# Performance work log

Hardware: AMD Instinct MI355X
Metric: run time of the kernel (lower is better)

The kernel has to match this reference:

```python
import jax, jax.numpy as jnp
import numpy as np

N_NODES = 50000
N_EDGES = 800000
N_GRAPHS = 128
IN_DIM = 12          # state_ndim + action_ndim
C = 64               # n_channels
N_LAYERS = 2
NEG_SLOPE = 0.01     # torch leaky_relu default


def setup_inputs() -> dict:
    key = jax.random.key(0)
    ks = jax.random.split(key, 16)
    state = jax.random.normal(ks[0], (N_NODES, 8), dtype=jnp.float32)
    action = jax.random.normal(ks[1], (N_NODES, 4), dtype=jnp.float32)
    edge_index = jax.random.randint(ks[2], (2, N_EDGES), 0, N_NODES, dtype=jnp.int64)
    edge_attr = jax.random.normal(ks[3], (N_EDGES, IN_DIM), dtype=jnp.float32)
    batch = jnp.sort(jax.random.randint(ks[4], (N_NODES,), 0, N_GRAPHS, dtype=jnp.int64))
    s = 0.05
    params = {
        "W_in": jax.random.normal(ks[5], (IN_DIM, C), dtype=jnp.float32) * s,
        "b_in": jnp.zeros((C,), dtype=jnp.float32),
        "W_self": jax.random.normal(ks[6], (N_LAYERS, C, C), dtype=jnp.float32) * s,
        "W_nbr": jax.random.normal(ks[7], (N_LAYERS, C, C), dtype=jnp.float32) * s,
        "W_edge": jax.random.normal(ks[8], (N_LAYERS, IN_DIM, C), dtype=jnp.float32) * s,
        "b_conv": jnp.zeros((N_LAYERS, C), dtype=jnp.float32),
        "W_out": jax.random.normal(ks[9], (C, 1), dtype=jnp.float32) * s,
        "b_out": jnp.zeros((1,), dtype=jnp.float32),
    }
    return {"state": state, "action": action, "edge_index": edge_index,
            "edge_attr": edge_attr, "batch": batch, **params}


def reference(state, action, edge_index, edge_attr, batch,
              W_in, b_in, W_self, W_nbr, W_edge, b_conv, W_out, b_out):
    N = state.shape[0]
    src, dst = edge_index[0], edge_index[1]
    act = lambda v: jax.nn.leaky_relu(v, NEG_SLOPE)

    # read-in: concat state/action -> node embedding [N, C]
    x = jnp.concatenate([state, action], axis=-1)
    h = act(x @ W_in + b_in)

    # message passing: gather -> transform -> scatter-add, edge_attr-conditioned
    for l in range(W_self.shape[0]):
        m = h[src] @ W_nbr[l] + edge_attr @ W_edge[l]          # [E, C]
        agg = jax.ops.segment_sum(m, dst, num_segments=N)      # [N, C]
        h = act(h @ W_self[l] + agg + b_conv[l])

    # read-out to scalar per node, then scatter_mean over graph ids
    y = h @ W_out + b_out                                      # [N, 1]
    sums = jax.ops.segment_sum(y, batch, num_segments=N_GRAPHS)
    counts = jax.ops.segment_sum(jnp.ones((N, 1), y.dtype), batch,
                                 num_segments=N_GRAPHS)
    return sums / jnp.maximum(counts, 1.0)                     # [B, 1]
```

## Files before the change

### kernel.cpp

```cpp
#include <hip/hip_runtime.h>

#define NN 50000
#define NE 800000
#define NG 128
#define IN_DIM 12
#define C 64
#define NEG_SLOPE 0.01f
#define SCAN_BLOCKS 196
#define NOWN 8
#define OWN_RANGE 6250
#define ESTRIPE 2048
#define NSTRIPES ((NE + ESTRIPE - 1) / ESTRIPE)

typedef short short8 __attribute__((ext_vector_type(8)));
typedef float f32x4 __attribute__((ext_vector_type(4)));
typedef unsigned int uint4v __attribute__((ext_vector_type(4)));

__device__ __forceinline__ float lrelu(float v) {
    return v > 0.f ? v : NEG_SLOPE * v;
}
__device__ __forceinline__ float bflo(uint32_t v) { return __uint_as_float(v << 16); }
__device__ __forceinline__ float bfhi(uint32_t v) { return __uint_as_float(v & 0xffff0000u); }
__device__ __forceinline__ unsigned short bf16r(float x) {
    uint32_t u = __float_as_uint(x);
    u += 0x7fffu + ((u >> 16) & 1u);
    return (unsigned short)(u >> 16);
}
__device__ __forceinline__ uint32_t pack_bf16(float lo, float hi) {
    return (uint32_t)bf16r(lo) | ((uint32_t)bf16r(hi) << 16);
}

__global__ void readin_kernel(const float* __restrict__ state,
                              const float* __restrict__ action,
                              const float* __restrict__ W_in,
                              const float* __restrict__ b_in,
                              uint32_t* __restrict__ hb) {
    __shared__ float sW[IN_DIM * C];
    __shared__ float sb[C];
    int tid = threadIdx.x;
    for (int i = tid; i < IN_DIM * C; i += blockDim.x) sW[i] = W_in[i];
    if (tid < C) sb[tid] = b_in[tid];
    __syncthreads();

    int node = blockIdx.x * (blockDim.x >> 6) + (tid >> 6);
    int c = tid & 63;
    if (node >= NN) return;

    float x[IN_DIM];
#pragma unroll
    for (int k = 0; k < 8; k++) x[k] = state[node * 8 + k];
#pragma unroll
    for (int k = 0; k < 4; k++) x[8 + k] = action[node * 4 + k];

    float acc = sb[c];
#pragma unroll
    for (int k = 0; k < IN_DIM; k++) acc += x[k] * sW[k * C + c];
    float res = lrelu(acc);
    float p = __shfl_xor(res, 1);
    if (!(c & 1)) hb[node * 32 + (c >> 1)] = pack_bf16(res, p);
}

__global__ void hist_part(const int* __restrict__ dst, int* __restrict__ deg) {
    int owner = blockIdx.x & (NOWN - 1);
    int stripe = blockIdx.x >> 3;
    int lo = owner * OWN_RANGE, hi = lo + OWN_RANGE;
    int base = stripe * ESTRIPE;
    int end = base + ESTRIPE; if (end > NE) end = NE;
    for (int e = base + threadIdx.x; e < end; e += 256) {
        int d = dst[e];
        if (d >= lo && d < hi) atomicAdd(&deg[d], 1);
    }
}

__global__ void scan1_kernel(const int* __restrict__ deg,
                             int* __restrict__ excl,
                             int* __restrict__ bsum) {
    __shared__ int tmp[256];
    int tid = threadIdx.x;
    int i = blockIdx.x * 256 + tid;
    int v = (i < NN) ? deg[i] : 0;
    tmp[tid] = v;
    __syncthreads();
    for (int off = 1; off < 256; off <<= 1) {
        int t = (tid >= off) ? tmp[tid - off] : 0;
        __syncthreads();
        tmp[tid] += t;
        __syncthreads();
    }
    if (i < NN) excl[i] = tmp[tid] - v;
    if (tid == 255) bsum[blockIdx.x] = tmp[255];
}

__global__ void scan23_kernel(const int* __restrict__ excl,
                              const int* __restrict__ bsum,
                              int* __restrict__ row_start,
                              int* __restrict__ cursor) {
    __shared__ int s_off;
    int tid = threadIdx.x;
    if (tid < 64) {
        int p = 0;
        for (int i = tid; i < blockIdx.x; i += 64) p += bsum[i];
#pragma unroll
        for (int off = 32; off; off >>= 1) p += __shfl_xor(p, off);
        if (tid == 0) s_off = p;
    }
    __syncthreads();
    int i = blockIdx.x * 256 + tid;
    if (i < NN) {
        int v = excl[i] + s_off;
        row_start[i] = v;
        cursor[i] = v;
    }
}

__global__ void fill_part(const int* __restrict__ src,
                          const int* __restrict__ dst,
                          int* __restrict__ cursor,
                          int2* __restrict__ csr2) {
    int owner = blockIdx.x & (NOWN - 1);
    int stripe = blockIdx.x >> 3;
    int lo = owner * OWN_RANGE, hi = lo + OWN_RANGE;
    int base = stripe * ESTRIPE;
    int end = base + ESTRIPE; if (end > NE) end = NE;
    for (int e = base + threadIdx.x; e < end; e += 256) {
        int d = dst[e];
        if (d >= lo && d < hi) {
            int slot = atomicAdd(&cursor[d], 1);
            csr2[slot] = make_int2(src[e], e);
        }
    }
}

__global__ void wprep_kernel(const float* __restrict__ W_self,
                             const float* __restrict__ W_nbr,
                             unsigned short* __restrict__ WT) {
    int idx = blockIdx.x * 256 + threadIdx.x;
    if (idx >= 2 * 64 * 128) return;
    int l = idx >> 13;
    int rem = idx & 8191;
    int col = rem >> 7;
    int k = rem & 127;
    float v = (k < C) ? W_self[l * C * C + k * C + col]
                      : W_nbr[l * C * C + (k - C) * C + col];
    WT[idx] = bf16r(v);
}

__global__ void agg_e_kernel(const float* __restrict__ edge_attr,
                             const int* __restrict__ row_start,
                             const int* __restrict__ deg,
                             const int2* __restrict__ csr2,
                             const float* __restrict__ W_edge,
                             const float* __restrict__ b_conv,
                             float* __restrict__ E0,
                             float* __restrict__ E1) {
    __shared__ float sWe0[IN_DIM * C];
    __shared__ float sWe1[IN_DIM * C];
    __shared__ float sb0[C];
    __shared__ float sb1[C];
    int tid = threadIdx.x;
    for (int i = tid; i < IN_DIM * C; i += blockDim.x) {
        sWe0[i] = W_edge[i];
        sWe1[i] = W_edge[IN_DIM * C + i];
    }
    if (tid < C) { sb0[tid] = b_conv[tid]; sb1[tid] = b_conv[C + tid]; }
    __syncthreads();

    int node = blockIdx.x * (blockDim.x >> 6) + (tid >> 6);
    int lane = tid & 63;
    int g = lane >> 4;
    int cc = lane & 15;
    if (node >= NN) return;
    int start = row_start[node], cnt = deg[node];

    int myeid = (lane < cnt) ? csr2[start + lane].y : 0;
    int nb = cnt < 64 ? cnt : 64;

    float acc = 0.f, acc2 = 0.f;
    int j = 0;
    for (; j + 8 <= nb; j += 8) {
        int e0 = __shfl(myeid, j + g);
        int e1 = __shfl(myeid, j + 4 + g);
        if (cc < IN_DIM) {
            acc  += edge_attr[e0 * IN_DIM + cc];
            acc2 += edge_attr[e1 * IN_DIM + cc];
        }
    }
    for (; j + 4 <= nb; j += 4) {
        int e0 = __shfl(myeid, j + g);
        if (cc < IN_DIM) acc += edge_attr[e0 * IN_DIM + cc];
    }
    {
        int e0 = __shfl(myeid, (j + g < 64) ? (j + g) : 0);
        if (j + g < nb && cc < IN_DIM) acc += edge_attr[e0 * IN_DIM + cc];
    }
    for (int i2 = 64 + g; i2 < cnt; i2 += 4) {
        int e = csr2[start + i2].y;
        if (cc < IN_DIM) acc += edge_attr[e * IN_DIM + cc];
    }
    acc += acc2;
    acc += __shfl_xor(acc, 16);
    acc += __shfl_xor(acc, 32);
    float e0v = sb0[lane];
    float e1v = sb1[lane];
#pragma unroll
    for (int k = 0; k < IN_DIM; k++) {
        float ak = __shfl(acc, k);
        e0v += ak * sWe0[k * C + lane];
        e1v += ak * sWe1[k * C + lane];
    }
    E0[node * C + lane] = e0v;
    E1[node * C + lane] = e1v;
}

__global__ void gather_kernel(const uint32_t* __restrict__ hb_in,
                              const int* __restrict__ row_start,
                              const int* __restrict__ deg,
                              const int2* __restrict__ csr2,
                              uint32_t* __restrict__ aggb) {
    int tid = threadIdx.x;
    int node = blockIdx.x * (blockDim.x >> 6) + (tid >> 6);
    int lane = tid & 63;
    if (node >= NN) return;

    int start = row_start[node], cnt = deg[node];
    int half = lane >> 5;
    int q = lane & 31;

    int myidx = (lane < cnt) ? csr2[start + lane].x : 0;
    int nb = cnt < 64 ? cnt : 64;

    float a0 = 0.f, a1 = 0.f, b0v = 0.f, b1v = 0.f;
    float c0 = 0.f, c1 = 0.f, d0 = 0.f, d1 = 0.f;
    int j = 0;
    for (; j + 16 <= nb; j += 16) {
        int p = j + 4 * half;
        int s0 = __shfl(myidx, p);
        int s1 = __shfl(myidx, p + 1);
        int s2 = __shfl(myidx, p + 2);
        int s3 = __shfl(myidx, p + 3);
        int s4 = __shfl(myidx, p + 8);
        int s5 = __shfl(myidx, p + 9);
        int s6 = __shfl(myidx, p + 10);
        int s7 = __shfl(myidx, p + 11);
        uint32_t v0 = hb_in[s0 * 32 + q];
        uint32_t v1 = hb_in[s1 * 32 + q];
        uint32_t v2 = hb_in[s2 * 32 + q];
        uint32_t v3 = hb_in[s3 * 32 + q];
        uint32_t v4 = hb_in[s4 * 32 + q];
        uint32_t v5 = hb_in[s5 * 32 + q];
        uint32_t v6 = hb_in[s6 * 32 + q];
        uint32_t v7 = hb_in[s7 * 32 + q];
        a0  += bflo(v0); a1  += bfhi(v0);
        b0v += bflo(v1); b1v += bfhi(v1);
        c0  += bflo(v2); c1  += bfhi(v2);
        d0  += bflo(v3); d1  += bfhi(v3);
        a0  += bflo(v4); a1  += bfhi(v4);
        b0v += bflo(v5); b1v += bfhi(v5);
        c0  += bflo(v6); c1  += bfhi(v6);
        d0  += bflo(v7); d1  += bfhi(v7);
    }
    for (; j + 8 <= nb; j += 8) {
        int p = j + 4 * half;
        int s0 = __shfl(myidx, p);
        int s1 = __shfl(myidx, p + 1);
        int s2 = __shfl(myidx, p + 2);
        int s3 = __shfl(myidx, p + 3);
        uint32_t v0 = hb_in[s0 * 32 + q];
        uint32_t v1 = hb_in[s1 * 32 + q];
        uint32_t v2 = hb_in[s2 * 32 + q];
        uint32_t v3 = hb_in[s3 * 32 + q];
        a0  += bflo(v0); a1  += bfhi(v0);
        b0v += bflo(v1); b1v += bfhi(v1);
        c0  += bflo(v2); c1  += bfhi(v2);
        d0  += bflo(v3); d1  += bfhi(v3);
    }
    for (; j + 2 <= nb; j += 2) {
        int s = __shfl(myidx, j + half);
        uint32_t v = hb_in[s * 32 + q];
        a0 += bflo(v); a1 += bfhi(v);
    }
    {
        int s = __shfl(myidx, (j < 64) ? j : 0);
        if (j < nb && half == 0) {
            uint32_t v = hb_in[s * 32 + q];
            a0 += bflo(v); a1 += bfhi(v);
        }
    }
    for (int i2 = 64 + half; i2 < cnt; i2 += 2) {
        int s = csr2[start + i2].x;
        uint32_t v = hb_in[s * 32 + q];
        a0 += bflo(v); a1 += bfhi(v);
    }
    a0 += b0v + c0 + d0;
    a1 += b1v + c1 + d1;
    a0 += __shfl_xor(a0, 32);
    a1 += __shfl_xor(a1, 32);
    if (lane < 32) aggb[node * 32 + q] = pack_bf16(a0, a1);
}

__global__ __launch_bounds__(512) void gemm_kernel(
        const uint32_t* __restrict__ hbA,
        const uint32_t* __restrict__ aggb,
        const unsigned short* __restrict__ WT,
        const float* __restrict__ E,
        unsigned short* __restrict__ hb_out) {
    int tid = threadIdx.x;
    int w = tid >> 6;
    int l = tid & 63;
    int mt = blockIdx.x * 2 + (w >> 2);
    if (mt * 16 >= NN) return;
    int nt = w & 3;
    int node_base = mt * 16;

    int arow = l & 15;
    int kg = l >> 4;
    int gcol = nt * 16 + arow;

    const uint32_t* aptr = hbA + (node_base + arow) * 32 + kg * 4;
    const uint32_t* gptr = aggb + (node_base + arow) * 32 + kg * 4;
    short8 a0 = __builtin_bit_cast(short8, *reinterpret_cast<const uint4v*>(aptr));
    short8 a1 = __builtin_bit_cast(short8, *reinterpret_cast<const uint4v*>(aptr + 16));
    short8 a2 = __builtin_bit_cast(short8, *reinterpret_cast<const uint4v*>(gptr));
    short8 a3 = __builtin_bit_cast(short8, *reinterpret_cast<const uint4v*>(gptr + 16));

    const unsigned short* bbase = WT + gcol * 128 + kg * 8;
    short8 b0 = __builtin_bit_cast(short8, *reinterpret_cast<const uint4v*>(bbase));
    short8 b1 = __builtin_bit_cast(short8, *reinterpret_cast<const uint4v*>(bbase + 32));
    short8 b2 = __builtin_bit_cast(short8, *reinterpret_cast<const uint4v*>(bbase + 64));
    short8 b3 = __builtin_bit_cast(short8, *reinterpret_cast<const uint4v*>(bbase + 96));

    f32x4 acc;
#pragma unroll
    for (int r = 0; r < 4; r++)
        acc[r] = E[(node_base + kg * 4 + r) * C + gcol];

    acc = __builtin_amdgcn_mfma_f32_16x16x32_bf16(a0, b0, acc, 0, 0, 0);
    acc = __builtin_amdgcn_mfma_f32_16x16x32_bf16(a1, b1, acc, 0, 0, 0);
    acc = __builtin_amdgcn_mfma_f32_16x16x32_bf16(a2, b2, acc, 0, 0, 0);
    acc = __builtin_amdgcn_mfma_f32_16x16x32_bf16(a3, b3, acc, 0, 0, 0);

#pragma unroll
    for (int r = 0; r < 4; r++) {
        float res = lrelu(acc[r]);
        hb_out[(node_base + kg * 4 + r) * C + gcol] = bf16r(res);
    }
}

__global__ void readout_fused(const unsigned short* __restrict__ hb,
                              const float* __restrict__ W_out,
                              const float* __restrict__ b_out,
                              const int* __restrict__ batch,
                              float* __restrict__ sums,
                              float* __restrict__ counts) {
    __shared__ float s_sum[NG];
    __shared__ float s_cnt[NG];
    int tid = threadIdx.x;
    if (tid < NG) { s_sum[tid] = 0.f; s_cnt[tid] = 0.f; }
    __syncthreads();

    int lane = tid & 63;
    int wave = tid >> 6;
    int base = blockIdx.x * 256 + wave * 64;
    float w = W_out[lane];
    float b0 = b_out[0];

    if (base < NN) {
        int last = base + 63;
        bool full = (last < NN);
        int gf = batch[base];
        int gl = batch[full ? last : (NN - 1)];
        if (full && gf == gl) {
            float p = 0.f;
            for (int i = 0; i < 64; i++)
                p += __uint_as_float((uint32_t)hb[(base + i) * C + lane] << 16);
            p *= w;
#pragma unroll
            for (int off = 32; off; off >>= 1) p += __shfl_xor(p, off);
            if (lane == 0) {
                atomicAdd(&s_sum[gf], p + 64.f * b0);
                atomicAdd(&s_cnt[gf], 64.f);
            }
        } else {
            float y_local = 0.f;
            for (int i = 0; i < 64; i++) {
                int nd = base + i;
                float v = 0.f;
                if (nd < NN) v = __uint_as_float((uint32_t)hb[nd * C + lane] << 16) * w;
#pragma unroll
                for (int off = 32; off; off >>= 1) v += __shfl_xor(v, off);
                if (lane == i) y_local = v + b0;
            }
            int nd = base + lane;
            if (nd < NN) {
                int g = batch[nd];
                atomicAdd(&s_sum[g], y_local);
                atomicAdd(&s_cnt[g], 1.0f);
            }
        }
    }
    __syncthreads();
    if (tid < NG && s_cnt[tid] != 0.f) {
        atomicAdd(&sums[tid], s_sum[tid]);
        atomicAdd(&counts[tid], s_cnt[tid]);
    }
}

__global__ void finalize_kernel(const float* __restrict__ sums,
                                const float* __restrict__ counts,
                                float* __restrict__ out) {
    int g = threadIdx.x;
    if (g < NG) out[g] = sums[g] / fmaxf(counts[g], 1.0f);
}

extern "C" void kernel_launch(void* const* d_in, const int* in_sizes, int n_in,
                              void* d_out, int out_size, void* d_ws, size_t ws_size,
                              hipStream_t stream) {
    const float* state     = (const float*)d_in[0];
    const float* action    = (const float*)d_in[1];
    const int*   edge_index= (const int*)d_in[2];
    const float* edge_attr = (const float*)d_in[3];
    const int*   batch     = (const int*)d_in[4];
    const float* W_in      = (const float*)d_in[5];
    const float* b_in      = (const float*)d_in[6];
    const float* W_self    = (const float*)d_in[7];
    const float* W_nbr     = (const float*)d_in[8];
    const float* W_edge    = (const float*)d_in[9];
    const float* b_conv    = (const float*)d_in[10];
    const float* W_out     = (const float*)d_in[11];
    const float* b_out     = (const float*)d_in[12];
    float* out = (float*)d_out;

    const int* src = edge_index;
    const int* dst = edge_index + NE;

    float* ws      = (float*)d_ws;
    float* E0      = ws;
    float* E1      = E0 + NN * C;
    float* sums    = E1 + NN * C;
    float* counts  = sums + NG;
    int*   deg     = (int*)(counts + NG);
    int*   excl    = deg + NN;
    int*   row_start = excl + NN;
    int*   cursor  = row_start + NN;
    int*   bsum    = cursor + NN;
    int2*  csr2    = (int2*)(bsum + 256);
    uint32_t* hb_a = (uint32_t*)(csr2 + NE);
    uint32_t* hb_b = hb_a + NN * 32;
    uint32_t* aggb = hb_b + NN * 32;
    unsigned short* WT = (unsigned short*)(aggb + NN * 32);

    hipMemsetAsync(deg, 0, NN * sizeof(int), stream);
    hipMemsetAsync(sums, 0, 2 * NG * sizeof(float), stream);

    const int THREADS = 256;
    int node_blocks = (NN + 3) / 4;
    int part_blocks = NSTRIPES * NOWN;

    readin_kernel<<<node_blocks, THREADS, 0, stream>>>(state, action, W_in, b_in, hb_a);

    hist_part<<<part_blocks, THREADS, 0, stream>>>(dst, deg);
    scan1_kernel<<<SCAN_BLOCKS, 256, 0, stream>>>(deg, excl, bsum);
    scan23_kernel<<<SCAN_BLOCKS, 256, 0, stream>>>(excl, bsum, row_start, cursor);
    fill_part<<<part_blocks, THREADS, 0, stream>>>(src, dst, cursor, csr2);

    wprep_kernel<<<64, 256, 0, stream>>>(W_self, W_nbr, WT);

    agg_e_kernel<<<node_blocks, THREADS, 0, stream>>>(
        edge_attr, row_start, deg, csr2, W_edge, b_conv, E0, E1);

    int gemm_blocks = (3125 + 1) / 2;

    gather_kernel<<<node_blocks, THREADS, 0, stream>>>(hb_a, row_start, deg, csr2, aggb);
    gemm_kernel<<<gemm_blocks, 512, 0, stream>>>(
        hb_a, aggb, WT, E0, (unsigned short*)hb_b);

    gather_kernel<<<node_blocks, THREADS, 0, stream>>>(hb_b, row_start, deg, csr2, aggb);
    gemm_kernel<<<gemm_blocks, 512, 0, stream>>>(
        hb_b, aggb, WT + 64 * 128, E1, (unsigned short*)hb_a);

    int ro_blocks = (NN + 255) / 256;
    readout_fused<<<ro_blocks, THREADS, 0, stream>>>(
        (const unsigned short*)hb_a, W_out, b_out, batch, sums, counts);
    finalize_kernel<<<1, 128, 0, stream>>>(sums, counts, out);
}
```

Measured before the change: 338.2 us.

## Fold edge-attribute projection into MFMA GEMM via bf16 CSR-ordered edge features

fill_part now converts each edge's 12 attributes to bf16 and writes them into a 32-byte record in CSR order, next to a separate source-index array. agg_e only sums these contiguous records per node into a 12-wide bf16 aggregate. The W_edge projection and bias move into the GEMM as a fifth MFMA step over an extended K dimension of 160. This removes the random edge_attr gather and the two fp32 [N,64] E buffers, at the cost of a larger CSR write in fill_part and bf16 rounding of the edge features and their sums.

Measured after the change: 335.6 us. No clear change (-0.8%).

```diff
diff --git a/kernel.cpp b/kernel.cpp
--- a/kernel.cpp
+++ b/kernel.cpp
@@ -5,6 +5,7 @@
 #define NG 128
 #define IN_DIM 12
 #define C 64
+#define KTOT 160
 #define NEG_SLOPE 0.01f
 #define SCAN_BLOCKS 196
 #define NOWN 8
@@ -115,8 +116,10 @@
 
 __global__ void fill_part(const int* __restrict__ src,
                           const int* __restrict__ dst,
+                          const float* __restrict__ edge_attr,
                           int* __restrict__ cursor,
-                          int2* __restrict__ csr2) {
+                          int* __restrict__ csr_src,
+                          uint4v* __restrict__ csr_ea) {
     int owner = blockIdx.x & (NOWN - 1);
     int stripe = blockIdx.x >> 3;
     int lo = owner * OWN_RANGE, hi = lo + OWN_RANGE;
@@ -126,96 +129,63 @@
         int d = dst[e];
         if (d >= lo && d < hi) {
             int slot = atomicAdd(&cursor[d], 1);
-            csr2[slot] = make_int2(src[e], e);
+            csr_src[slot] = src[e];
+            const float4* ea = reinterpret_cast<const float4*>(edge_attr + e * IN_DIM);
+            float4 f0 = ea[0], f1 = ea[1], f2 = ea[2];
+            uint4v w0, w1;
+            w0[0] = pack_bf16(f0.x, f0.y); w0[1] = pack_bf16(f0.z, f0.w);
+            w0[2] = pack_bf16(f1.x, f1.y); w0[3] = pack_bf16(f1.z, f1.w);
+            w1[0] = pack_bf16(f2.x, f2.y); w1[1] = pack_bf16(f2.z, f2.w);
+            w1[2] = 0u; w1[3] = 0u;
+            csr_ea[slot * 2] = w0;
+            csr_ea[slot * 2 + 1] = w1;
         }
     }
 }
 
 __global__ void wprep_kernel(const float* __restrict__ W_self,
                              const float* __restrict__ W_nbr,
+                             const float* __restrict__ W_edge,
                              unsigned short* __restrict__ WT) {
     int idx = blockIdx.x * 256 + threadIdx.x;
-    if (idx >= 2 * 64 * 128) return;
-    int l = idx >> 13;
-    int rem = idx & 8191;
-    int col = rem >> 7;
-    int k = rem & 127;
-    float v = (k < C) ? W_self[l * C * C + k * C + col]
-                      : W_nbr[l * C * C + (k - C) * C + col];
+    if (idx >= 2 * C * KTOT) return;
+    int l = idx / (C * KTOT);
+    int rem = idx % (C * KTOT);
+    int col = rem / KTOT;
+    int k = rem % KTOT;
+    float v = 0.f;
+    if (k < C)                    v = W_self[l * C * C + k * C + col];
+    else if (k < 2 * C)           v = W_nbr[l * C * C + (k - C) * C + col];
+    else if (k < 2 * C + IN_DIM)  v = W_edge[l * IN_DIM * C + (k - 2 * C) * C + col];
     WT[idx] = bf16r(v);
 }
 
-__global__ void agg_e_kernel(const float* __restrict__ edge_attr,
+__global__ void agg_e_kernel(const uint32_t* __restrict__ csr_ea,
                              const int* __restrict__ row_start,
                              const int* __restrict__ deg,
-                             const int2* __restrict__ csr2,
-                             const float* __restrict__ W_edge,
-                             const float* __restrict__ b_conv,
-                             float* __restrict__ E0,
-                             float* __restrict__ E1) {
-    __shared__ float sWe0[IN_DIM * C];
-    __shared__ float sWe1[IN_DIM * C];
-    __shared__ float sb0[C];
-    __shared__ float sb1[C];
-    int tid = threadIdx.x;
-    for (int i = tid; i < IN_DIM * C; i += blockDim.x) {
-        sWe0[i] = W_edge[i];
-        sWe1[i] = W_edge[IN_DIM * C + i];
-    }
-    if (tid < C) { sb0[tid] = b_conv[tid]; sb1[tid] = b_conv[C + tid]; }
-    __syncthreads();
-
+                             uint32_t* __restrict__ aggeb) {
+    int tid = threadIdx.x;
     int node = blockIdx.x * (blockDim.x >> 6) + (tid >> 6);
     int lane = tid & 63;
-    int g = lane >> 4;
-    int cc = lane & 15;
     if (node >= NN) return;
     int start = row_start[node], cnt = deg[node];
-
-    int myeid = (lane < cnt) ? csr2[start + lane].y : 0;
-    int nb = cnt < 64 ? cnt : 64;
-
-    float acc = 0.f, acc2 = 0.f;
-    int j = 0;
-    for (; j + 8 <= nb; j += 8) {
-        int e0 = __shfl(myeid, j + g);
-        int e1 = __shfl(myeid, j + 4 + g);
-        if (cc < IN_DIM) {
-            acc  += edge_attr[e0 * IN_DIM + cc];
-            acc2 += edge_attr[e1 * IN_DIM + cc];
-        }
-    }
-    for (; j + 4 <= nb; j += 4) {
-        int e0 = __shfl(myeid, j + g);
-        if (cc < IN_DIM) acc += edge_attr[e0 * IN_DIM + cc];
-    }
-    {
-        int e0 = __shfl(myeid, (j + g < 64) ? (j + g) : 0);
-        if (j + g < nb && cc < IN_DIM) acc += edge_attr[e0 * IN_DIM + cc];
-    }
-    for (int i2 = 64 + g; i2 < cnt; i2 += 4) {
-        int e = csr2[start + i2].y;
-        if (cc < IN_DIM) acc += edge_attr[e * IN_DIM + cc];
-    }
-    acc += acc2;
-    acc += __shfl_xor(acc, 16);
-    acc += __shfl_xor(acc, 32);
-    float e0v = sb0[lane];
-    float e1v = sb1[lane];
-#pragma unroll
-    for (int k = 0; k < IN_DIM; k++) {
-        float ak = __shfl(acc, k);
-        e0v += ak * sWe0[k * C + lane];
-        e1v += ak * sWe1[k * C + lane];
-    }
-    E0[node * C + lane] = e0v;
-    E1[node * C + lane] = e1v;
+    int eg = lane >> 3;
+    int comp = lane & 7;
+    float s0 = 0.f, s1 = 0.f;
+    for (int j = eg; j < cnt; j += 8) {
+        uint32_t v = csr_ea[(size_t)(start + j) * 8 + comp];
+        s0 += bflo(v); s1 += bfhi(v);
+    }
+    s0 += __shfl_xor(s0, 8);  s1 += __shfl_xor(s1, 8);
+    s0 += __shfl_xor(s0, 16); s1 += __shfl_xor(s1, 16);
+    s0 += __shfl_xor(s0, 32); s1 += __shfl_xor(s1, 32);
+    if (lane < 8) aggeb[node * 8 + comp] = pack_bf16(s0, s1);
 }
 
 __global__ void gather_kernel(const uint32_t* __restrict__ hb_in,
                               const int* __restrict__ row_start,
                               const int* __restrict__ deg,
-                              const int2* __restrict__ csr2,
+                              const int* __restrict__ csr_src,
                               uint32_t* __restrict__ aggb) {
     int tid = threadIdx.x;
     int node = blockIdx.x * (blockDim.x >> 6) + (tid >> 6);
@@ -226,7 +196,7 @@
     int half = lane >> 5;
     int q = lane & 31;
 
-    int myidx = (lane < cnt) ? csr2[start + lane].x : 0;
+    int myidx = (lane < cnt) ? csr_src[start + lane] : 0;
     int nb = cnt < 64 ? cnt : 64;
 
     float a0 = 0.f, a1 = 0.f, b0v = 0.f, b1v = 0.f;
@@ -287,7 +257,7 @@
         }
     }
     for (int i2 = 64 + half; i2 < cnt; i2 += 2) {
-        int s = csr2[start + i2].x;
+        int s = csr_src[start + i2];
         uint32_t v = hb_in[s * 32 + q];
         a0 += bflo(v); a1 += bfhi(v);
     }
@@ -301,8 +271,9 @@
 __global__ __launch_bounds__(512) void gemm_kernel(
         const uint32_t* __restrict__ hbA,
         const uint32_t* __restrict__ aggb,
+        const uint32_t* __restrict__ aggeb,
         const unsigned short* __restrict__ WT,
-        const float* __restrict__ E,
+        const float* __restrict__ bias,
         unsigned short* __restrict__ hb_out) {
     int tid = threadIdx.x;
     int w = tid >> 6;
@@ -322,22 +293,26 @@
     short8 a1 = __builtin_bit_cast(short8, *reinterpret_cast<const uint4v*>(aptr + 16));
     short8 a2 = __builtin_bit_cast(short8, *reinterpret_cast<const uint4v*>(gptr));
     short8 a3 = __builtin_bit_cast(short8, *reinterpret_cast<const uint4v*>(gptr + 16));
-
-    const unsigned short* bbase = WT + gcol * 128 + kg * 8;
+    short8 a4 = {0, 0, 0, 0, 0, 0, 0, 0};
+    if (kg < 2)
+        a4 = __builtin_bit_cast(short8, *reinterpret_cast<const uint4v*>(
+                 aggeb + (node_base + arow) * 8 + kg * 4));
+
+    const unsigned short* bbase = WT + gcol * KTOT + kg * 8;
     short8 b0 = __builtin_bit_cast(short8, *reinterpret_cast<const uint4v*>(bbase));
     short8 b1 = __builtin_bit_cast(short8, *reinterpret_cast<const uint4v*>(bbase + 32));
     short8 b2 = __builtin_bit_cast(short8, *reinterpret_cast<const uint4v*>(bbase + 64));
     short8 b3 = __builtin_bit_cast(short8, *reinterpret_cast<const uint4v*>(bbase + 96));
-
-    f32x4 acc;
-#pragma unroll
-    for (int r = 0; r < 4; r++)
-        acc[r] = E[(node_base + kg * 4 + r) * C + gcol];
+    short8 b4 = __builtin_bit_cast(short8, *reinterpret_cast<const uint4v*>(bbase + 128));
+
+    float bv = bias[gcol];
+    f32x4 acc = {bv, bv, bv, bv};
 
     acc = __builtin_amdgcn_mfma_f32_16x16x32_bf16(a0, b0, acc, 0, 0, 0);
     acc = __builtin_amdgcn_mfma_f32_16x16x32_bf16(a1, b1, acc, 0, 0, 0);
     acc = __builtin_amdgcn_mfma_f32_16x16x32_bf16(a2, b2, acc, 0, 0, 0);
     acc = __builtin_amdgcn_mfma_f32_16x16x32_bf16(a3, b3, acc, 0, 0, 0);
+    acc = __builtin_amdgcn_mfma_f32_16x16x32_bf16(a4, b4, acc, 0, 0, 0);
 
 #pragma unroll
     for (int r = 0; r < 4; r++) {
@@ -434,20 +409,20 @@
     const int* dst = edge_index + NE;
 
     float* ws      = (float*)d_ws;
-    float* E0      = ws;
-    float* E1      = E0 + NN * C;
-    float* sums    = E1 + NN * C;
+    float* sums    = ws;
     float* counts  = sums + NG;
     int*   deg     = (int*)(counts + NG);
     int*   excl    = deg + NN;
     int*   row_start = excl + NN;
     int*   cursor  = row_start + NN;
     int*   bsum    = cursor + NN;
-    int2*  csr2    = (int2*)(bsum + 256);
-    uint32_t* hb_a = (uint32_t*)(csr2 + NE);
+    int*   csr_src = bsum + 256;
+    uint32_t* csr_ea = (uint32_t*)(csr_src + NE);
+    uint32_t* hb_a = csr_ea + (size_t)NE * 8;
     uint32_t* hb_b = hb_a + NN * 32;
     uint32_t* aggb = hb_b + NN * 32;
-    unsigned short* WT = (unsigned short*)(aggb + NN * 32);
+    uint32_t* aggeb = aggb + NN * 32;
+    unsigned short* WT = (unsigned short*)(aggeb + NN * 8);
 
     hipMemsetAsync(deg, 0, NN * sizeof(int), stream);
     hipMemsetAsync(sums, 0, 2 * NG * sizeof(float), stream);
@@ -461,22 +436,22 @@
     hist_part<<<part_blocks, THREADS, 0, stream>>>(dst, deg);
     scan1_kernel<<<SCAN_BLOCKS, 256, 0, stream>>>(deg, excl, bsum);
     scan23_kernel<<<SCAN_BLOCKS, 256, 0, stream>>>(excl, bsum, row_start, cursor);
-    fill_part<<<part_blocks, THREADS, 0, stream>>>(src, dst, cursor, csr2);
-
-    wprep_kernel<<<64, 256, 0, stream>>>(W_self, W_nbr, WT);
-
-    agg_e_kernel<<<node_blocks, THREADS, 0, stream>>>(
-        edge_attr, row_start, deg, csr2, W_edge, b_conv, E0, E1);
+    fill_part<<<part_blocks, THREADS, 0, stream>>>(src, dst, edge_attr, cursor,
+                                                   csr_src, (uint4v*)csr_ea);
+
+    wprep_kernel<<<80, 256, 0, stream>>>(W_self, W_nbr, W_edge, WT);
+
+    agg_e_kernel<<<node_blocks, THREADS, 0, stream>>>(csr_ea, row_start, deg, aggeb);
 
     int gemm_blocks = (3125 + 1) / 2;
 
-    gather_kernel<<<node_blocks, THREADS, 0, stream>>>(hb_a, row_start, deg, csr2, aggb);
+    gather_kernel<<<node_blocks, THREADS, 0, stream>>>(hb_a, row_start, deg, csr_src, aggb);
     gemm_kernel<<<gemm_blocks, 512, 0, stream>>>(
-        hb_a, aggb, WT, E0, (unsigned short*)hb_b);
-
-    gather_kernel<<<node_blocks, THREADS, 0, stream>>>(hb_b, row_start, deg, csr2, aggb);
+        hb_a, aggb, aggeb, WT, b_conv, (unsigned short*)hb_b);
+
+    gather_kernel<<<node_blocks, THREADS, 0, stream>>>(hb_b, row_start, deg, csr_src, aggb);
     gemm_kernel<<<gemm_blocks, 512, 0, stream>>>(
-        hb_b, aggb, WT + 64 * 128, E1, (unsigned short*)hb_a);
+        hb_b, aggb, aggeb, WT + C * KTOT, b_conv + C, (unsigned short*)hb_a);
 
     int ro_blocks = (NN + 255) / 256;
     readout_fused<<<ro_blocks, THREADS, 0, stream>>>(
```
